# Optimization experiments

Measured on AMD Instinct MI355X. Metric: run time of the kernel, lower is better.

Reference implementation:

```python
import jax, jax.numpy as jnp
import numpy as np


def _squash(t):
    # squash along axis=2 (the atoms axis of [B, D, A, 1, 1])
    norm = jnp.linalg.norm(t, axis=2, keepdims=True)
    n2 = norm * norm
    return t / norm * (n2 / (1.0 + n2))


def setup_inputs() -> dict:
    key = jax.random.key(0)
    k1, k2 = jax.random.split(key)
    B, I, Ain, D, A = 32, 2048, 16, 32, 16
    x = jax.random.normal(k1, (B, I, Ain, 1, 1), jnp.float32)
    weights = 0.1 * jax.random.normal(k2, (I, Ain, D * A, 1, 1), jnp.float32)
    bias = jnp.full((D, A, 1, 1), 0.1, jnp.float32)  # nn.init.constant_(0.1)
    return {"x": x, "weights": weights, "bias": bias, "num_routing": 3}


def reference(x, weights, bias, num_routing):
    B, I, Ain = x.shape[:3]
    D, A = bias.shape[:2]
    # Vote computation (standard voting): sum over input_atoms.
    # Torch does expand+mul+sum; einsum is the same math without the 4.8GB intermediate.
    votes = jnp.einsum('bia,iao->bio', x[:, :, :, 0, 0],
                       weights[:, :, :, 0, 0]).reshape(B, I, D, A, 1, 1)
    votes_sg = jax.lax.stop_gradient(votes)  # votes_trans_stopped in torch
    logits = jnp.zeros((B, I, D, 1, 1), x.dtype)
    activation = None
    for i in range(num_routing):
        route = jax.nn.softmax(logits, axis=2)  # [B, I, D, 1, 1], softmax over D
        v = votes if i == num_routing - 1 else votes_sg
        # route broadcast over atoms axis; sum over input capsules I
        preact = jnp.sum(route[:, :, :, None] * v, axis=1) + bias  # [B, D, A, 1, 1]
        activation = _squash(preact)
        if i < num_routing - 1:
            # agreement update uses non-stopped votes (as in torch)
            logits = logits + jnp.sum(votes * activation[:, None], axis=3)  # [B, I, D, 1, 1]
    return activation
```

## Files before the change

### kernel.cpp

```cpp
#include <hip/hip_runtime.h>


#define B_  32
#define I_  2048
#define K_  16
#define O_  512

#define GLB(p)  ((const __attribute__((address_space(1))) void*)(p))
#define LDSP(p) ((__attribute__((address_space(3))) void*)(p))

__global__ __launch_bounds__(512)
void votes_kernel(const float* __restrict__ x, const float* __restrict__ W,
                  float* __restrict__ votes)
{
    const int tid  = threadIdx.x;
    const int lane = tid & 63;
    const int wave = tid >> 6;
    const int i    = blockIdx.x;

    const int wv    = __builtin_amdgcn_readfirstlane(wave);
    const int bbase = wv * 4;

    __shared__ float sW[K_ * O_];

    {
        const char* gb = (const char*)(W + (size_t)i * (K_ * O_));
        #pragma unroll
        for (int c = 0; c < 4; ++c) {
            const int s = c * 512 + tid;
            const int f = ((s >> 10) & 1) | ((s & 1) << 1)
                        | (((s >> 1) & 31) << 2) | (((s >> 6) & 15) << 7);
            __builtin_amdgcn_global_load_lds(GLB(gb + (f << 4)),
                LDSP(&sW[(c * 512 + wave * 64) * 4]), 16, 0, 0);
        }
    }

    float xs[4][16];
    #pragma unroll
    for (int bb = 0; bb < 4; ++bb) {
        const float4* xp = (const float4*)(x + ((size_t)(bbase + bb) * I_ + i) * K_);
        #pragma unroll
        for (int q = 0; q < 4; ++q) {
            float4 v = xp[q];
            xs[bb][4*q+0]=v.x; xs[bb][4*q+1]=v.y; xs[bb][4*q+2]=v.z; xs[bb][4*q+3]=v.w;
        }
    }

    __syncthreads();

    float V[4][8];
    #pragma unroll
    for (int bb = 0; bb < 4; ++bb)
        #pragma unroll
        for (int j = 0; j < 8; ++j) V[bb][j] = 0.f;
    #pragma unroll
    for (int k = 0; k < K_; ++k) {
        const float4 w0 = *(const float4*)&sW[k * 256 + lane * 4];
        const float4 w1 = *(const float4*)&sW[4096 + k * 256 + lane * 4];
        const float w[8] = {w0.x, w0.y, w0.z, w0.w, w1.x, w1.y, w1.z, w1.w};
        #pragma unroll
        for (int bb = 0; bb < 4; ++bb) {
            const float xb = xs[bb][k];
            #pragma unroll
            for (int j = 0; j < 8; ++j) V[bb][j] = fmaf(xb, w[j], V[bb][j]);
        }
    }

    #pragma unroll
    for (int bb = 0; bb < 4; ++bb) {
        float4* dst = (float4*)(votes + ((size_t)i * B_ + bbase + bb) * O_ + lane * 8);
        dst[0] = make_float4(V[bb][0], V[bb][1], V[bb][2], V[bb][3]);
        dst[1] = make_float4(V[bb][4], V[bb][5], V[bb][6], V[bb][7]);
    }
}

template<int PASS>
__global__ __launch_bounds__(256)
void route_kernel(const float* __restrict__ votes, const float* __restrict__ act0,
                  const float* __restrict__ act1, float* __restrict__ partial)
{
    const int tid  = threadIdx.x;
    const int lane = tid & 63;
    const int wave = tid >> 6;
    const int b    = blockIdx.x & 31;
    const int ic   = blockIdx.x >> 5;
    const int i0   = ic * 32 + wave * 8;

    float as_[8];
    {
        const float4* p = (const float4*)(act0 + b * O_ + lane * 8);
        float4 f0 = p[0], f1 = p[1];
        as_[0]=f0.x; as_[1]=f0.y; as_[2]=f0.z; as_[3]=f0.w;
        as_[4]=f1.x; as_[5]=f1.y; as_[6]=f1.z; as_[7]=f1.w;
        if (PASS == 2) {
            const float4* q = (const float4*)(act1 + b * O_ + lane * 8);
            float4 g0 = q[0], g1 = q[1];
            as_[0]+=g0.x; as_[1]+=g0.y; as_[2]+=g0.z; as_[3]+=g0.w;
            as_[4]+=g1.x; as_[5]+=g1.y; as_[6]+=g1.z; as_[7]+=g1.w;
        }
    }

    float facc[8];
    #pragma unroll
    for (int j = 0; j < 8; ++j) facc[j] = 0.f;

    #pragma unroll
    for (int ii = 0; ii < 8; ++ii) {
        const float4* vp = (const float4*)(votes + ((size_t)(i0 + ii) * B_ + b) * O_ + lane * 8);
        const float4 v0 = vp[0], v1 = vp[1];
        const float V[8] = {v0.x, v0.y, v0.z, v0.w, v1.x, v1.y, v1.z, v1.w};
        float p0 = 0.f;
        #pragma unroll
        for (int j = 0; j < 8; ++j) p0 = fmaf(V[j], as_[j], p0);
        p0 += __shfl_xor(p0, 1);
        const float e = __expf(p0);
        float s = e;
        s += __shfl_xor(s, 2);
        s += __shfl_xor(s, 4);
        s += __shfl_xor(s, 8);
        s += __shfl_xor(s, 16);
        s += __shfl_xor(s, 32);
        const float r = e * __builtin_amdgcn_rcpf(s);
        #pragma unroll
        for (int j = 0; j < 8; ++j) facc[j] = fmaf(r, V[j], facc[j]);
    }

    float4* dst = (float4*)(partial + ((size_t)(ic * 4 + wave) * B_ + b) * O_ + lane * 8);
    dst[0] = make_float4(facc[0], facc[1], facc[2], facc[3]);
    dst[1] = make_float4(facc[4], facc[5], facc[6], facc[7]);
}

__global__ __launch_bounds__(256)
void reduce_squash(const float* __restrict__ partial, const float* __restrict__ bias,
                   float scale, int nw, float* __restrict__ out)
{
    const int t   = threadIdx.x;
    const int g4  = blockIdx.x * 8 + (t & 7);
    const int sl  = t >> 3;
    const int per = nw >> 5;
    const float4* p4 = (const float4*)partial;
    float4 s = make_float4(0.f, 0.f, 0.f, 0.f);
    #pragma unroll 8
    for (int w = sl * per; w < sl * per + per; ++w) {
        const float4 v = p4[(size_t)w * (B_ * O_ / 4) + g4];
        s.x += v.x; s.y += v.y; s.z += v.z; s.w += v.w;
    }
    __shared__ float4 red[256];
    red[t] = s;
    __syncthreads();
    if (t < 8) {
        float4 v = red[t];
        #pragma unroll
        for (int r = 1; r < 32; ++r) {
            const float4 u = red[t + 8 * r];
            v.x += u.x; v.y += u.y; v.z += u.z; v.w += u.w;
        }
        const float4 bi = ((const float4*)bias)[g4 & 127];
        float4 p;
        p.x = fmaf(v.x, scale, bi.x);
        p.y = fmaf(v.y, scale, bi.y);
        p.z = fmaf(v.z, scale, bi.z);
        p.w = fmaf(v.w, scale, bi.w);
        float nn = p.x*p.x + p.y*p.y + p.z*p.z + p.w*p.w;
        nn += __shfl_xor(nn, 1);
        nn += __shfl_xor(nn, 2);
        const float sc = sqrtf(nn) / (1.f + nn);
        p.x *= sc; p.y *= sc; p.z *= sc; p.w *= sc;
        ((float4*)out)[g4] = p;
    }
}

extern "C" void kernel_launch(void* const* d_in, const int* in_sizes, int n_in,
                              void* d_out, int out_size, void* d_ws, size_t ws_size,
                              hipStream_t stream) {
    const float* x    = (const float*)d_in[0];
    const float* W    = (const float*)d_in[1];
    const float* bias = (const float*)d_in[2];
    float* out = (float*)d_out;

    float* votes   = (float*)d_ws;
    float* partial = votes + (size_t)I_ * B_ * O_;
    float* act0    = partial + (size_t)256 * B_ * O_;
    float* act1    = act0 + B_ * O_;

    votes_kernel<<<I_, 512, 0, stream>>>(x, W, votes);
    reduce_squash<<<512, 256, 0, stream>>>(votes, bias, 1.f / 32.f, I_, act0);
    route_kernel<1><<<2048, 256, 0, stream>>>(votes, act0, nullptr, partial);
    reduce_squash<<<512, 256, 0, stream>>>(partial, bias, 1.f, 256, act1);
    route_kernel<2><<<2048, 256, 0, stream>>>(votes, act0, act1, partial);
    reduce_squash<<<512, 256, 0, stream>>>(partial, bias, 1.f, 256, out);
}
```

Before: 217.6 us.

## Rewrite votes kernel with register-held weights, b-major layout, fused first-pass partial sums

The votes kernel now gives each block four input capsules, keeps their weights in registers instead of staging through LDS, and loops over the batch. It writes votes in [B, I, O] order and also emits per-group partial sums over I. The first reduce therefore reads 512 partial slices instead of the full 2048-row votes tensor. Route kernels index the new layout. The cost is an extra partial-sum buffer write, scalar rather than vector stores, and fewer blocks (512), which may lower parallelism.

After: 267.0 us. 1.23x slower.

```diff
diff --git a/kernel.cpp b/kernel.cpp
--- a/kernel.cpp
+++ b/kernel.cpp
@@ -5,72 +5,49 @@
 #define I_  2048
 #define K_  16
 #define O_  512
-
-#define GLB(p)  ((const __attribute__((address_space(1))) void*)(p))
-#define LDSP(p) ((__attribute__((address_space(3))) void*)(p))
+#define IC_ 4
+#define NGV 512
+#define NGR 256
 
 __global__ __launch_bounds__(512)
 void votes_kernel(const float* __restrict__ x, const float* __restrict__ W,
-                  float* __restrict__ votes)
+                  float* __restrict__ votes, float* __restrict__ pr0)
 {
-    const int tid  = threadIdx.x;
-    const int lane = tid & 63;
-    const int wave = tid >> 6;
-    const int i    = blockIdx.x;
+    const int t  = threadIdx.x;
+    const int g  = blockIdx.x;
+    const int i0 = g * IC_;
 
-    const int wv    = __builtin_amdgcn_readfirstlane(wave);
-    const int bbase = wv * 4;
+    float w[IC_][K_];
+    #pragma unroll
+    for (int ii = 0; ii < IC_; ++ii)
+        #pragma unroll
+        for (int k = 0; k < K_; ++k)
+            w[ii][k] = W[((size_t)(i0 + ii) * K_ + k) * O_ + t];
 
-    __shared__ float sW[K_ * O_];
-
-    {
-        const char* gb = (const char*)(W + (size_t)i * (K_ * O_));
+    #pragma unroll 2
+    for (int b = 0; b < B_; ++b) {
+        float xs[IC_][K_];
+        {
+            const float4* xp = (const float4*)(x + ((size_t)b * I_ + i0) * K_);
+            #pragma unroll
+            for (int q = 0; q < 16; ++q) {
+                const float4 v = xp[q];
+                xs[q >> 2][4*(q & 3) + 0] = v.x;
+                xs[q >> 2][4*(q & 3) + 1] = v.y;
+                xs[q >> 2][4*(q & 3) + 2] = v.z;
+                xs[q >> 2][4*(q & 3) + 3] = v.w;
+            }
+        }
+        float facc = 0.f;
         #pragma unroll
-        for (int c = 0; c < 4; ++c) {
-            const int s = c * 512 + tid;
-            const int f = ((s >> 10) & 1) | ((s & 1) << 1)
-                        | (((s >> 1) & 31) << 2) | (((s >> 6) & 15) << 7);
-            __builtin_amdgcn_global_load_lds(GLB(gb + (f << 4)),
-                LDSP(&sW[(c * 512 + wave * 64) * 4]), 16, 0, 0);
+        for (int ii = 0; ii < IC_; ++ii) {
+            float V = 0.f;
+            #pragma unroll
+            for (int k = 0; k < K_; ++k) V = fmaf(xs[ii][k], w[ii][k], V);
+            votes[((size_t)b * I_ + i0 + ii) * O_ + t] = V;
+            facc += V;
         }
-    }
-
-    float xs[4][16];
-    #pragma unroll
-    for (int bb = 0; bb < 4; ++bb) {
-        const float4* xp = (const float4*)(x + ((size_t)(bbase + bb) * I_ + i) * K_);
-        #pragma unroll
-        for (int q = 0; q < 4; ++q) {
-            float4 v = xp[q];
-            xs[bb][4*q+0]=v.x; xs[bb][4*q+1]=v.y; xs[bb][4*q+2]=v.z; xs[bb][4*q+3]=v.w;
-        }
-    }
-
-    __syncthreads();
-
-    float V[4][8];
-    #pragma unroll
-    for (int bb = 0; bb < 4; ++bb)
-        #pragma unroll
-        for (int j = 0; j < 8; ++j) V[bb][j] = 0.f;
-    #pragma unroll
-    for (int k = 0; k < K_; ++k) {
-        const float4 w0 = *(const float4*)&sW[k * 256 + lane * 4];
-        const float4 w1 = *(const float4*)&sW[4096 + k * 256 + lane * 4];
-        const float w[8] = {w0.x, w0.y, w0.z, w0.w, w1.x, w1.y, w1.z, w1.w};
-        #pragma unroll
-        for (int bb = 0; bb < 4; ++bb) {
-            const float xb = xs[bb][k];
-            #pragma unroll
-            for (int j = 0; j < 8; ++j) V[bb][j] = fmaf(xb, w[j], V[bb][j]);
-        }
-    }
-
-    #pragma unroll
-    for (int bb = 0; bb < 4; ++bb) {
-        float4* dst = (float4*)(votes + ((size_t)i * B_ + bbase + bb) * O_ + lane * 8);
-        dst[0] = make_float4(V[bb][0], V[bb][1], V[bb][2], V[bb][3]);
-        dst[1] = make_float4(V[bb][4], V[bb][5], V[bb][6], V[bb][7]);
+        pr0[((size_t)g * B_ + b) * O_ + t] = facc;
     }
 }
 
@@ -106,7 +83,7 @@
 
     #pragma unroll
     for (int ii = 0; ii < 8; ++ii) {
-        const float4* vp = (const float4*)(votes + ((size_t)(i0 + ii) * B_ + b) * O_ + lane * 8);
+        const float4* vp = (const float4*)(votes + ((size_t)b * I_ + i0 + ii) * O_ + lane * 8);
         const float4 v0 = vp[0], v1 = vp[1];
         const float V[8] = {v0.x, v0.y, v0.z, v0.w, v1.x, v1.y, v1.z, v1.w};
         float p0 = 0.f;
@@ -179,14 +156,15 @@
     float* out = (float*)d_out;
 
     float* votes   = (float*)d_ws;
-    float* partial = votes + (size_t)I_ * B_ * O_;
-    float* act0    = partial + (size_t)256 * B_ * O_;
+    float* pr0     = votes + (size_t)B_ * I_ * O_;
+    float* partial = pr0 + (size_t)NGV * B_ * O_;
+    float* act0    = partial + (size_t)NGR * B_ * O_;
     float* act1    = act0 + B_ * O_;
 
-    votes_kernel<<<I_, 512, 0, stream>>>(x, W, votes);
-    reduce_squash<<<512, 256, 0, stream>>>(votes, bias, 1.f / 32.f, I_, act0);
+    votes_kernel<<<NGV, 512, 0, stream>>>(x, W, votes, pr0);
+    reduce_squash<<<512, 256, 0, stream>>>(pr0, bias, 1.f / 32.f, NGV, act0);
     route_kernel<1><<<2048, 256, 0, stream>>>(votes, act0, nullptr, partial);
-    reduce_squash<<<512, 256, 0, stream>>>(partial, bias, 1.f, 256, act1);
+    reduce_squash<<<512, 256, 0, stream>>>(partial, bias, 1.f, NGR, act1);
     route_kernel<2><<<2048, 256, 0, stream>>>(votes, act0, act1, partial);
-    reduce_squash<<<512, 256, 0, stream>>>(partial, bias, 1.f, 256, out);
+    reduce_squash<<<512, 256, 0, stream>>>(partial, bias, 1.f, NGR, out);
 }
```
